# Kernel optimization log

Measured on AMD Instinct MI355X. Metric: run time of the kernel, lower is better.

The kernel has to match this reference:

```python
import jax, jax.numpy as jnp
import numpy as np

B, H, T, S, D, V = 4, 16, 512, 512, 1024, 32000
EPS = 1e-12


def setup_inputs() -> dict:
    key = jax.random.key(0)
    ks = jax.random.split(key, 12)
    return {
        "decoder_attention": jax.random.uniform(ks[0], (B, H, T, S), dtype=jnp.float32),
        "decoder_last_hidden_state": jax.random.normal(ks[1], (B, T, D), dtype=jnp.float32),
        "enc_input_ids": jax.random.randint(ks[2], (B, S), 0, V, dtype=jnp.int64),
        "logits": jax.random.normal(ks[3], (B, T, V), dtype=jnp.float32),
        "decoder_input_embeds": jax.random.normal(ks[4], (B, T, D), dtype=jnp.float32),
        "encoder_last_hidden_state": jax.random.normal(ks[5], (B, S, D), dtype=jnp.float32),
        # Linear(d_model, 1) params (weight as [D] vector, scalar bias)
        "w_logits": jax.random.normal(ks[6], (D,), dtype=jnp.float32) / np.sqrt(D),
        "b_logits": jnp.zeros((), dtype=jnp.float32),
        "w_embeds": jax.random.normal(ks[7], (D,), dtype=jnp.float32) / np.sqrt(D),
        "b_embeds": jnp.zeros((), dtype=jnp.float32),
        "w_enc": jax.random.normal(ks[8], (D,), dtype=jnp.float32) / np.sqrt(D),
        "b_enc": jnp.zeros((), dtype=jnp.float32),
        "bias": jnp.zeros((), dtype=jnp.float32),
    }


def reference(decoder_attention, decoder_last_hidden_state, enc_input_ids, logits,
              decoder_input_embeds, encoder_last_hidden_state,
              w_logits, b_logits, w_embeds, b_embeds, w_enc, b_enc, bias):
    g_distribution = jax.nn.softmax(logits, axis=-1)                      # [B,T,V]
    c_attention = jnp.mean(decoder_attention, axis=1)                      # [B,T,S]

    # scatter_add attention into vocab space: c_dist[b,t,enc_ids[b,s]] += c_attn[b,t,s]
    b_idx = jnp.arange(B)[:, None, None]
    t_idx = jnp.arange(T)[None, :, None]
    v_idx = enc_input_ids[:, None, :]                                      # [B,1,S]
    c_distribution = jnp.zeros_like(g_distribution).at[b_idx, t_idx, v_idx].add(c_attention)

    ctx = jnp.einsum('bts,bsd->btd', c_attention, encoder_last_hidden_state)  # [B,T,D]
    gate_logit = (decoder_last_hidden_state @ w_logits + b_logits
                  + decoder_input_embeds @ w_embeds + b_embeds
                  + ctx @ w_enc + b_enc + bias)                             # [B,T]
    p_copy = jax.nn.sigmoid(gate_logit)[..., None]                          # [B,T,1]

    mixed = p_copy * c_distribution + (1.0 - p_copy) * g_distribution
    return jnp.log(mixed + EPS)
```

## Files before the change

### kernel.cpp

```cpp
#include <hip/hip_runtime.h>
#include <math.h>

constexpr int NB = 4;
constexpr int NH = 16;
constexpr int NT = 512;
constexpr int NS = 512;
constexpr int ND = 1024;
constexpr int NV = 32000;
constexpr float EPS = 1e-12f;

__global__ void mean_h_kernel(const float* __restrict__ A, float* __restrict__ c_att) {
    const int S4 = NS / 4;
    int idx = blockIdx.x * blockDim.x + threadIdx.x;
    if (idx >= NB * NT * S4) return;
    int s4 = idx % S4;
    int bt = idx / S4;
    int b = bt / NT;
    int t = bt % NT;
    const float4* A4 = (const float4*)A;
    float4 acc = make_float4(0.f, 0.f, 0.f, 0.f);
#pragma unroll
    for (int h = 0; h < NH; ++h) {
        float4 v = A4[((size_t)(b * NH + h) * NT + t) * S4 + s4];
        acc.x += v.x; acc.y += v.y; acc.z += v.z; acc.w += v.w;
    }
    const float inv = 1.0f / NH;
    float4 r;
    r.x = acc.x * inv; r.y = acc.y * inv; r.z = acc.z * inv; r.w = acc.w * inv;
    ((float4*)c_att)[(size_t)bt * S4 + s4] = r;
}

__global__ void eproj_kernel(const float* __restrict__ E, const float* __restrict__ w_enc,
                             float* __restrict__ e_proj) {
    int gid = blockIdx.x * blockDim.x + threadIdx.x;
    int w = gid >> 6;
    int lane = gid & 63;
    if (w >= NB * NS) return;
    const float4* e4 = (const float4*)(E + (size_t)w * ND);
    const float4* w4 = (const float4*)w_enc;
    float acc = 0.f;
#pragma unroll
    for (int i = lane; i < ND / 4; i += 64) {
        float4 a = e4[i], b = w4[i];
        acc += a.x * b.x + a.y * b.y + a.z * b.z + a.w * b.w;
    }
    for (int off = 32; off > 0; off >>= 1) acc += __shfl_down(acc, off, 64);
    if (lane == 0) e_proj[w] = acc;
}

__global__ void gate_kernel(const float* __restrict__ dlhs, const float* __restrict__ die,
                            const float* __restrict__ c_att, const float* __restrict__ e_proj,
                            const float* __restrict__ w_logits, const float* __restrict__ w_embeds,
                            const float* __restrict__ b_logits, const float* __restrict__ b_embeds,
                            const float* __restrict__ b_enc, const float* __restrict__ bias,
                            float* __restrict__ p_copy) {
    int gid = blockIdx.x * blockDim.x + threadIdx.x;
    int row = gid >> 6;
    int lane = gid & 63;
    if (row >= NB * NT) return;
    const float4* x1 = (const float4*)(dlhs + (size_t)row * ND);
    const float4* w1 = (const float4*)w_logits;
    const float4* x2 = (const float4*)(die + (size_t)row * ND);
    const float4* w2 = (const float4*)w_embeds;
    float acc = 0.f;
#pragma unroll
    for (int i = lane; i < ND / 4; i += 64) {
        float4 a = x1[i], b = w1[i];
        acc += a.x * b.x + a.y * b.y + a.z * b.z + a.w * b.w;
        float4 c = x2[i], d = w2[i];
        acc += c.x * d.x + c.y * d.y + c.z * d.z + c.w * d.w;
    }
    int bidx = row / NT;
    const float4* ca = (const float4*)(c_att + (size_t)row * NS);
    const float4* ep = (const float4*)(e_proj + (size_t)bidx * NS);
#pragma unroll
    for (int i = lane; i < NS / 4; i += 64) {
        float4 a = ca[i], b = ep[i];
        acc += a.x * b.x + a.y * b.y + a.z * b.z + a.w * b.w;
    }
    for (int off = 32; off > 0; off >>= 1) acc += __shfl_down(acc, off, 64);
    if (lane == 0) {
        float g = acc + b_logits[0] + b_embeds[0] + b_enc[0] + bias[0];
        p_copy[row] = 1.f / (1.f + __expf(-g));
    }
}

constexpr int HSIZE = 2048;

__global__ __launch_bounds__(1024) void out_kernel(
    const float* __restrict__ logits, const int* __restrict__ ids,
    const float* __restrict__ c_att, const float* __restrict__ p_copy,
    float* __restrict__ out) {
    __shared__ int hkey[HSIZE];
    __shared__ float hval[HSIZE];
    __shared__ float sred[16];

    const int row = blockIdx.x;
    const int tid = threadIdx.x;
    const int b = row / NT;

    for (int i = tid; i < HSIZE; i += 1024) {
        hkey[i] = -1;
        hval[i] = 0.f;
    }

    const float4* L4 = (const float4*)(logits + (size_t)row * NV);
    float ssum = 0.f;
    for (int i = tid; i < NV / 4; i += 1024) {
        float4 x = L4[i];
        ssum += __expf(x.x) + __expf(x.y) + __expf(x.z) + __expf(x.w);
    }
    for (int off = 32; off > 0; off >>= 1) ssum += __shfl_down(ssum, off, 64);
    const int wave = tid >> 6;
    const int lane = tid & 63;
    if (lane == 0) sred[wave] = ssum;
    __syncthreads();
    if (tid == 0) {
        float z = 0.f;
#pragma unroll
        for (int i = 0; i < 16; ++i) z += sred[i];
        sred[0] = z;
    }
    __syncthreads();
    const float Z = sred[0];

    for (int s = tid; s < NS; s += 1024) {
        int id = ids[b * NS + s];
        float wgt = c_att[(size_t)row * NS + s];
        unsigned h = ((unsigned)id * 2654435761u) >> 21;
        while (true) {
            int prev = atomicCAS(&hkey[h], -1, id);
            if (prev == -1 || prev == id) {
                atomicAdd(&hval[h], wgt);
                break;
            }
            h = (h + 1) & (HSIZE - 1);
        }
    }
    __syncthreads();

    const float p = p_copy[row];
    const float a = (1.f - p) / Z;

    float4* O4 = (float4*)(out + (size_t)row * NV);
    for (int i = tid; i < NV / 4; i += 1024) {
        float4 x = L4[i];
        float4 y;
        y.x = __logf(fmaf(a, __expf(x.x), EPS));
        y.y = __logf(fmaf(a, __expf(x.y), EPS));
        y.z = __logf(fmaf(a, __expf(x.z), EPS));
        y.w = __logf(fmaf(a, __expf(x.w), EPS));
        O4[i] = y;
    }
    __syncthreads();

    for (int i = tid; i < HSIZE; i += 1024) {
        int id = hkey[i];
        if (id >= 0) {
            float x = logits[(size_t)row * NV + id];
            out[(size_t)row * NV + id] = __logf(a * __expf(x) + p * hval[i] + EPS);
        }
    }
}

extern "C" void kernel_launch(void* const* d_in, const int* in_sizes, int n_in,
                              void* d_out, int out_size, void* d_ws, size_t ws_size,
                              hipStream_t stream) {
    const float* dec_attn = (const float*)d_in[0];
    const float* dlhs     = (const float*)d_in[1];
    const int*   ids      = (const int*)d_in[2];
    const float* logits   = (const float*)d_in[3];
    const float* die      = (const float*)d_in[4];
    const float* enc      = (const float*)d_in[5];
    const float* w_logits = (const float*)d_in[6];
    const float* b_logits = (const float*)d_in[7];
    const float* w_embeds = (const float*)d_in[8];
    const float* b_embeds = (const float*)d_in[9];
    const float* w_enc    = (const float*)d_in[10];
    const float* b_enc    = (const float*)d_in[11];
    const float* bias     = (const float*)d_in[12];
    float* out = (float*)d_out;

    char* ws = (char*)d_ws;
    float* c_att  = (float*)ws;
    float* e_proj = (float*)(ws + (size_t)NB * NT * NS * 4);
    float* p_copy = e_proj + NB * NS;

    {
        int n = NB * NT * (NS / 4);
        mean_h_kernel<<<n / 256, 256, 0, stream>>>(dec_attn, c_att);
    }
    {
        int waves = NB * NS;
        eproj_kernel<<<(waves * 64) / 256, 256, 0, stream>>>(enc, w_enc, e_proj);
    }
    {
        int waves = NB * NT;
        gate_kernel<<<(waves * 64) / 256, 256, 0, stream>>>(
            dlhs, die, c_att, e_proj, w_logits, w_embeds,
            b_logits, b_embeds, b_enc, bias, p_copy);
    }
    {
        out_kernel<<<NB * NT, 1024, 0, stream>>>(logits, ids, c_att, p_copy, out);
    }
}
```

Before: 561.3 us.

## Fuse head-mean and gate computation into per-row output kernel with smaller blocks

The head-mean and gate kernels are folded into the per-row output kernel. Each 256-thread block computes its row's attention mean into shared memory, the gate dot products and the softmax denominator, then writes the output. This drops the c_att and p_copy round trips through global memory and two launches. The non-copied path now uses an algebraic shortcut, log(a*exp(x)) = x + log(a), when the result is above -20, which avoids exp/log per element. The cost is slightly different rounding near that threshold.

```diff
diff --git a/kernel.cpp b/kernel.cpp
--- a/kernel.cpp
+++ b/kernel.cpp
@@ -8,27 +8,6 @@
 constexpr int ND = 1024;
 constexpr int NV = 32000;
 constexpr float EPS = 1e-12f;
-
-__global__ void mean_h_kernel(const float* __restrict__ A, float* __restrict__ c_att) {
-    const int S4 = NS / 4;
-    int idx = blockIdx.x * blockDim.x + threadIdx.x;
-    if (idx >= NB * NT * S4) return;
-    int s4 = idx % S4;
-    int bt = idx / S4;
-    int b = bt / NT;
-    int t = bt % NT;
-    const float4* A4 = (const float4*)A;
-    float4 acc = make_float4(0.f, 0.f, 0.f, 0.f);
-#pragma unroll
-    for (int h = 0; h < NH; ++h) {
-        float4 v = A4[((size_t)(b * NH + h) * NT + t) * S4 + s4];
-        acc.x += v.x; acc.y += v.y; acc.z += v.z; acc.w += v.w;
-    }
-    const float inv = 1.0f / NH;
-    float4 r;
-    r.x = acc.x * inv; r.y = acc.y * inv; r.z = acc.z * inv; r.w = acc.w * inv;
-    ((float4*)c_att)[(size_t)bt * S4 + s4] = r;
-}
 
 __global__ void eproj_kernel(const float* __restrict__ E, const float* __restrict__ w_enc,
                              float* __restrict__ e_proj) {
@@ -48,87 +27,77 @@
     if (lane == 0) e_proj[w] = acc;
 }
 
-__global__ void gate_kernel(const float* __restrict__ dlhs, const float* __restrict__ die,
-                            const float* __restrict__ c_att, const float* __restrict__ e_proj,
-                            const float* __restrict__ w_logits, const float* __restrict__ w_embeds,
-                            const float* __restrict__ b_logits, const float* __restrict__ b_embeds,
-                            const float* __restrict__ b_enc, const float* __restrict__ bias,
-                            float* __restrict__ p_copy) {
-    int gid = blockIdx.x * blockDim.x + threadIdx.x;
-    int row = gid >> 6;
-    int lane = gid & 63;
-    if (row >= NB * NT) return;
-    const float4* x1 = (const float4*)(dlhs + (size_t)row * ND);
-    const float4* w1 = (const float4*)w_logits;
-    const float4* x2 = (const float4*)(die + (size_t)row * ND);
-    const float4* w2 = (const float4*)w_embeds;
-    float acc = 0.f;
-#pragma unroll
-    for (int i = lane; i < ND / 4; i += 64) {
-        float4 a = x1[i], b = w1[i];
-        acc += a.x * b.x + a.y * b.y + a.z * b.z + a.w * b.w;
-        float4 c = x2[i], d = w2[i];
-        acc += c.x * d.x + c.y * d.y + c.z * d.z + c.w * d.w;
-    }
-    int bidx = row / NT;
-    const float4* ca = (const float4*)(c_att + (size_t)row * NS);
-    const float4* ep = (const float4*)(e_proj + (size_t)bidx * NS);
-#pragma unroll
-    for (int i = lane; i < NS / 4; i += 64) {
-        float4 a = ca[i], b = ep[i];
-        acc += a.x * b.x + a.y * b.y + a.z * b.z + a.w * b.w;
-    }
-    for (int off = 32; off > 0; off >>= 1) acc += __shfl_down(acc, off, 64);
-    if (lane == 0) {
-        float g = acc + b_logits[0] + b_embeds[0] + b_enc[0] + bias[0];
-        p_copy[row] = 1.f / (1.f + __expf(-g));
-    }
-}
+constexpr int HSIZE = 2048;
+constexpr int BLK = 256;
 
-constexpr int HSIZE = 2048;
-
-__global__ __launch_bounds__(1024) void out_kernel(
-    const float* __restrict__ logits, const int* __restrict__ ids,
-    const float* __restrict__ c_att, const float* __restrict__ p_copy,
+__global__ __launch_bounds__(256, 8) void out_kernel(
+    const float* __restrict__ A,
+    const float* __restrict__ logits,
+    const int*   __restrict__ ids,
+    const float* __restrict__ dlhs,
+    const float* __restrict__ die,
+    const float* __restrict__ e_proj,
+    const float* __restrict__ w_logits, const float* __restrict__ w_embeds,
+    const float* __restrict__ b_logits, const float* __restrict__ b_embeds,
+    const float* __restrict__ b_enc, const float* __restrict__ bias,
     float* __restrict__ out) {
-    __shared__ int hkey[HSIZE];
+    __shared__ int   hkey[HSIZE];
     __shared__ float hval[HSIZE];
-    __shared__ float sred[16];
+    __shared__ float catt[NS];
+    __shared__ float sred[12];
 
     const int row = blockIdx.x;
     const int tid = threadIdx.x;
     const int b = row / NT;
+    const int t = row % NT;
 
-    for (int i = tid; i < HSIZE; i += 1024) {
+    for (int i = tid; i < HSIZE; i += BLK) {
         hkey[i] = -1;
         hval[i] = 0.f;
     }
 
-    const float4* L4 = (const float4*)(logits + (size_t)row * NV);
-    float ssum = 0.f;
-    for (int i = tid; i < NV / 4; i += 1024) {
-        float4 x = L4[i];
-        ssum += __expf(x.x) + __expf(x.y) + __expf(x.z) + __expf(x.w);
-    }
-    for (int off = 32; off > 0; off >>= 1) ssum += __shfl_down(ssum, off, 64);
-    const int wave = tid >> 6;
-    const int lane = tid & 63;
-    if (lane == 0) sred[wave] = ssum;
-    __syncthreads();
-    if (tid == 0) {
-        float z = 0.f;
-#pragma unroll
-        for (int i = 0; i < 16; ++i) z += sred[i];
-        sred[0] = z;
+    if (tid < NS / 4) {
+        const float4* A4 = (const float4*)A;
+        const size_t plane = (size_t)NT * (NS / 4);
+        size_t base = ((size_t)(b * NH) * NT + t) * (NS / 4) + tid;
+        float4 acc = make_float4(0.f, 0.f, 0.f, 0.f);
+#pragma unroll 4
+        for (int h = 0; h < NH; ++h) {
+            float4 v = A4[base + (size_t)h * plane];
+            acc.x += v.x; acc.y += v.y; acc.z += v.z; acc.w += v.w;
+        }
+        const float inv = 1.0f / NH;
+        ((float4*)catt)[tid] = make_float4(acc.x * inv, acc.y * inv, acc.z * inv, acc.w * inv);
     }
     __syncthreads();
-    const float Z = sred[0];
 
-    for (int s = tid; s < NS; s += 1024) {
+    const float4* L4 = (const float4*)(logits + (size_t)row * NV);
+    float zsum = 0.f;
+    for (int i = tid; i < NV / 4; i += BLK) {
+        float4 x = L4[i];
+        zsum += __expf(x.x) + __expf(x.y) + __expf(x.z) + __expf(x.w);
+    }
+
+    float gsum = 0.f;
+    {
+        const float4* x1 = (const float4*)(dlhs + (size_t)row * ND);
+        const float4* w1 = (const float4*)w_logits;
+        const float4* x2 = (const float4*)(die + (size_t)row * ND);
+        const float4* w2 = (const float4*)w_embeds;
+        float4 a0 = x1[tid], b0 = w1[tid];
+        gsum += a0.x * b0.x + a0.y * b0.y + a0.z * b0.z + a0.w * b0.w;
+        float4 a1 = x2[tid], b1 = w2[tid];
+        gsum += a1.x * b1.x + a1.y * b1.y + a1.z * b1.z + a1.w * b1.w;
+        const float* ep = e_proj + (size_t)b * NS;
+        gsum += catt[2 * tid] * ep[2 * tid];
+        gsum += catt[2 * tid + 1] * ep[2 * tid + 1];
+    }
+
+    for (int s = tid; s < NS; s += BLK) {
         int id = ids[b * NS + s];
-        float wgt = c_att[(size_t)row * NS + s];
+        float wgt = catt[s];
         unsigned h = ((unsigned)id * 2654435761u) >> 21;
-        while (true) {
+        for (int probe = 0; probe < HSIZE; ++probe) {
             int prev = atomicCAS(&hkey[h], -1, id);
             if (prev == -1 || prev == id) {
                 atomicAdd(&hval[h], wgt);
@@ -137,24 +106,44 @@
             h = (h + 1) & (HSIZE - 1);
         }
     }
+
+    for (int off = 32; off > 0; off >>= 1) {
+        zsum += __shfl_down(zsum, off, 64);
+        gsum += __shfl_down(gsum, off, 64);
+    }
+    const int wave = tid >> 6;
+    const int lane = tid & 63;
+    if (lane == 0) { sred[wave] = zsum; sred[4 + wave] = gsum; }
     __syncthreads();
-
-    const float p = p_copy[row];
-    const float a = (1.f - p) / Z;
+    if (tid == 0) {
+        float Z = sred[0] + sred[1] + sred[2] + sred[3];
+        float G = sred[4] + sred[5] + sred[6] + sred[7]
+                + b_logits[0] + b_embeds[0] + b_enc[0] + bias[0];
+        float p = 1.f / (1.f + __expf(-G));
+        float a = (1.f - p) / Z;
+        sred[8] = a;
+        sred[9] = p;
+        sred[10] = __logf(a);
+    }
+    __syncthreads();
+    const float a = sred[8];
+    const float p = sred[9];
+    const float la = sred[10];
 
     float4* O4 = (float4*)(out + (size_t)row * NV);
-    for (int i = tid; i < NV / 4; i += 1024) {
+    for (int i = tid; i < NV / 4; i += BLK) {
         float4 x = L4[i];
         float4 y;
-        y.x = __logf(fmaf(a, __expf(x.x), EPS));
-        y.y = __logf(fmaf(a, __expf(x.y), EPS));
-        y.z = __logf(fmaf(a, __expf(x.z), EPS));
-        y.w = __logf(fmaf(a, __expf(x.w), EPS));
+        float tx;
+        tx = x.x + la; y.x = (tx > -20.f) ? tx : __logf(__expf(tx) + EPS);
+        tx = x.y + la; y.y = (tx > -20.f) ? tx : __logf(__expf(tx) + EPS);
+        tx = x.z + la; y.z = (tx > -20.f) ? tx : __logf(__expf(tx) + EPS);
+        tx = x.w + la; y.w = (tx > -20.f) ? tx : __logf(__expf(tx) + EPS);
         O4[i] = y;
     }
     __syncthreads();
 
-    for (int i = tid; i < HSIZE; i += 1024) {
+    for (int i = tid; i < HSIZE; i += BLK) {
         int id = hkey[i];
         if (id >= 0) {
             float x = logits[(size_t)row * NV + id];
@@ -181,26 +170,15 @@
     const float* bias     = (const float*)d_in[12];
     float* out = (float*)d_out;
 
-    char* ws = (char*)d_ws;
-    float* c_att  = (float*)ws;
-    float* e_proj = (float*)(ws + (size_t)NB * NT * NS * 4);
-    float* p_copy = e_proj + NB * NS;
+    float* e_proj = (float*)d_ws;
 
-    {
-        int n = NB * NT * (NS / 4);
-        mean_h_kernel<<<n / 256, 256, 0, stream>>>(dec_attn, c_att);
-    }
     {
         int waves = NB * NS;
         eproj_kernel<<<(waves * 64) / 256, 256, 0, stream>>>(enc, w_enc, e_proj);
     }
     {
-        int waves = NB * NT;
-        gate_kernel<<<(waves * 64) / 256, 256, 0, stream>>>(
-            dlhs, die, c_att, e_proj, w_logits, w_embeds,
-            b_logits, b_embeds, b_enc, bias, p_copy);
-    }
-    {
-        out_kernel<<<NB * NT, 1024, 0, stream>>>(logits, ids, c_att, p_copy, out);
+        out_kernel<<<NB * NT, BLK, 0, stream>>>(
+            dec_attn, logits, ids, dlhs, die, e_proj,
+            w_logits, w_embeds, b_logits, b_embeds, b_enc, bias, out);
     }
 }
```

After: 613.8 us. 9.4% more time.
